# Kernel optimization log

Hardware: AMD Instinct MI355X
Metric: run time of the kernel (lower is better)

Reference implementation:

```python
import jax, jax.numpy as jnp
import numpy as np

N_NODES = 100000
N_EDGES = 1000000
D = 64


def _deg_inv_sqrt(idx, n):
    deg = jax.ops.segment_sum(jnp.ones(idx.shape[0], jnp.float32), idx, num_segments=n)
    deg = jnp.maximum(deg, 1.0)  # DGL clamps zero degrees to 1
    return jax.lax.rsqrt(deg)


def _graph_conv(x, W, b, src, dst, out_norm, in_norm):
    # norm='both': h = D_in^{-1/2} A D_out^{-1/2} x W + b
    h = x * out_norm[:, None]
    agg = jax.ops.segment_sum(h[src], dst, num_segments=x.shape[0])
    agg = agg * in_norm[:, None]
    return agg @ W + b


def setup_inputs() -> dict:
    key = jax.random.key(0)
    ks = jax.random.split(key, 8)
    x = jax.random.normal(ks[0], (N_NODES, D), dtype=jnp.float32)
    src = jax.random.randint(ks[1], (N_EDGES,), 0, N_NODES, dtype=jnp.int32)
    dst = jax.random.randint(ks[2], (N_EDGES,), 0, N_NODES, dtype=jnp.int32)
    s = 1.0 / np.sqrt(D)
    W1 = jax.random.normal(ks[3], (D, D), dtype=jnp.float32) * s
    W2 = jax.random.normal(ks[4], (D, D), dtype=jnp.float32) * s
    W3 = jax.random.normal(ks[5], (D, D), dtype=jnp.float32) * s
    b1 = jnp.zeros((D,), jnp.float32)
    b2 = jnp.zeros((D,), jnp.float32)
    b3 = jnp.zeros((D,), jnp.float32)
    return {"x": x, "src": src, "dst": dst,
            "W1": W1, "b1": b1, "W2": W2, "b2": b2, "W3": W3, "b3": b3}


def reference(x, src, dst, W1, b1, W2, b2, W3, b3):
    n = x.shape[0]
    out_norm = _deg_inv_sqrt(src, n)  # source out-degree norm
    in_norm = _deg_inv_sqrt(dst, n)   # dest in-degree norm
    h = _graph_conv(x, W1, b1, src, dst, out_norm, in_norm)
    h = jax.nn.relu(h)
    h = _graph_conv(h, W2, b2, src, dst, out_norm, in_norm)
    h = jax.nn.relu(h)
    h = _graph_conv(h, W3, b3, src, dst, out_norm, in_norm)
    return h
```

## Files before the change

kernel.cpp:

```cpp
#include <hip/hip_runtime.h>
#include <hip/hip_fp16.h>

#define D 64
#define SZ 512
#define EPB 4096
#define CAPB 8192

static __device__ __forceinline__ __half2 u2h2(unsigned u) {
    union { unsigned u; __half2 h; } c; c.u = u; return c.h;
}
static __device__ __forceinline__ unsigned h22u(__half2 h) {
    union { __half2 h; unsigned u; } c; c.h = h; return c.u;
}

__global__ __launch_bounds__(256) void scatter_kernel(
    const int* __restrict__ src, const int* __restrict__ dst,
    int* __restrict__ gcntD, int* __restrict__ gcntS,
    unsigned* __restrict__ packD, unsigned short* __restrict__ packS,
    int E, int nb) {
    int tid = threadIdx.x;
    __shared__ int hD[256], hS[256], baseD[256], baseS[256], curD[256], curS[256];
    hD[tid] = 0; hS[tid] = 0; curD[tid] = 0; curS[tid] = 0;
    __syncthreads();
    int ebase = (int)blockIdx.x * EPB;
#pragma unroll
    for (int k = 0; k < EPB / 256; k++) {
        int e = ebase + k * 256 + tid;
        if (e < E) {
            atomicAdd(&hD[dst[e] >> 9], 1);
            atomicAdd(&hS[src[e] >> 9], 1);
        }
    }
    __syncthreads();
    if (tid < nb) {
        int c = hD[tid];
        baseD[tid] = tid * CAPB + (c ? atomicAdd(&gcntD[tid], c) : 0);
        c = hS[tid];
        baseS[tid] = tid * CAPB + (c ? atomicAdd(&gcntS[tid], c) : 0);
    }
    __syncthreads();
#pragma unroll
    for (int k = 0; k < EPB / 256; k++) {
        int e = ebase + k * 256 + tid;
        if (e < E) {
            int s = src[e], d = dst[e];
            int bd = d >> 9, bs_ = s >> 9;
            int ld = atomicAdd(&curD[bd], 1);
            int ls = atomicAdd(&curS[bs_], 1);
            packD[baseD[bd] + ld] = ((unsigned)s << 9) | (unsigned)(d & 511);
            packS[baseS[bs_] + ls] = (unsigned short)(s & 511);
        }
    }
}

__global__ __launch_bounds__(256) void build_kernel(
    const unsigned* __restrict__ packD, const unsigned short* __restrict__ packS,
    const int* __restrict__ gcntD, const int* __restrict__ gcntS,
    int* __restrict__ csr, int* __restrict__ rowbeg, int* __restrict__ rowend,
    float* __restrict__ in_norm, float* __restrict__ out_norm,
    int n, int nb) {
    int tid = threadIdx.x;
    __shared__ int cnt[512], lptr[512], tmp[256];
    bool roleD = ((int)blockIdx.x < nb);
    int b = roleD ? (int)blockIdx.x : (int)blockIdx.x - nb;
    int bs = b * CAPB;
    int be = bs + (roleD ? gcntD[b] : gcntS[b]);
    cnt[tid] = 0; cnt[tid + 256] = 0;
    __syncthreads();
    if (roleD) {
        for (int i = bs + tid; i < be; i += 256)
            atomicAdd(&cnt[packD[i] & 511], 1);
        __syncthreads();
        int a0 = cnt[2 * tid], a1 = cnt[2 * tid + 1];
        tmp[tid] = a0 + a1; __syncthreads();
        for (int off = 1; off < 256; off <<= 1) {
            int u = (tid >= off) ? tmp[tid - off] : 0; __syncthreads();
            tmp[tid] += u; __syncthreads();
        }
        int ex = tmp[tid] - (a0 + a1);
        lptr[2 * tid] = ex; lptr[2 * tid + 1] = ex + a0;
        __syncthreads();
        int v0 = b * SZ + tid, v1 = v0 + 256;
        if (v0 < n) {
            rowbeg[v0] = bs + lptr[tid];
            rowend[v0] = bs + lptr[tid] + cnt[tid];
            in_norm[v0] = rsqrtf((float)max(cnt[tid], 1));
        }
        if (v1 < n) {
            rowbeg[v1] = bs + lptr[tid + 256];
            rowend[v1] = bs + lptr[tid + 256] + cnt[tid + 256];
            in_norm[v1] = rsqrtf((float)max(cnt[tid + 256], 1));
        }
        __syncthreads();
        for (int i = bs + tid; i < be; i += 256) {
            unsigned p = packD[i];
            int slot = atomicAdd(&lptr[p & 511], 1);
            csr[bs + slot] = (int)(p >> 9);
        }
    } else {
        for (int i = bs + tid; i < be; i += 256)
            atomicAdd(&cnt[packS[i]], 1);
        __syncthreads();
        int v0 = b * SZ + tid, v1 = v0 + 256;
        if (v0 < n) out_norm[v0] = rsqrtf((float)max(cnt[tid], 1));
        if (v1 < n) out_norm[v1] = rsqrtf((float)max(cnt[tid + 256], 1));
    }
}

template <int SCALE>
__global__ __launch_bounds__(256, 4) void gemm_kernel(
    const float* __restrict__ X, const float* __restrict__ W,
    const float* __restrict__ scale, __half* __restrict__ P, int n) {
    __shared__ float Ws[64 * 64];
    __shared__ float Xs[64 * 64];
    int tid = threadIdx.x;
    int row0 = (int)blockIdx.x * 64;
    if (row0 >= n) return;
    {
        const float4* W4 = (const float4*)W;
        float4* Ws4 = (float4*)Ws;
#pragma unroll
        for (int i = 0; i < 4; i++) Ws4[tid + 256 * i] = W4[tid + 256 * i];
    }
    {
#pragma unroll
        for (int i = 0; i < 4; i++) {
            int idx = tid + 256 * i;
            int r = idx >> 4, kq = idx & 15;
            float4 v = make_float4(0.f, 0.f, 0.f, 0.f);
            int row = row0 + r;
            if (row < n) v = ((const float4*)X)[(size_t)row * 16 + kq];
            *(float4*)&Xs[r * 64 + ((kq ^ (r & 15)) << 2)] = v;
        }
    }
    __syncthreads();

    int tx = tid & 15, ty = tid >> 4;
    float acc[4][4] = {};
#pragma unroll 4
    for (int kc = 0; kc < 16; kc++) {
        float4 wv[4];
#pragma unroll
        for (int j = 0; j < 4; j++) wv[j] = *(float4*)&Ws[(4 * kc + j) * 64 + 4 * tx];
#pragma unroll
        for (int r = 0; r < 4; r++) {
            int row = 4 * ty + r;
            float4 xv = *(float4*)&Xs[row * 64 + ((kc ^ (row & 15)) << 2)];
            acc[r][0] = fmaf(xv.x, wv[0].x, acc[r][0]);
            acc[r][1] = fmaf(xv.x, wv[0].y, acc[r][1]);
            acc[r][2] = fmaf(xv.x, wv[0].z, acc[r][2]);
            acc[r][3] = fmaf(xv.x, wv[0].w, acc[r][3]);
            acc[r][0] = fmaf(xv.y, wv[1].x, acc[r][0]);
            acc[r][1] = fmaf(xv.y, wv[1].y, acc[r][1]);
            acc[r][2] = fmaf(xv.y, wv[1].z, acc[r][2]);
            acc[r][3] = fmaf(xv.y, wv[1].w, acc[r][3]);
            acc[r][0] = fmaf(xv.z, wv[2].x, acc[r][0]);
            acc[r][1] = fmaf(xv.z, wv[2].y, acc[r][1]);
            acc[r][2] = fmaf(xv.z, wv[2].z, acc[r][2]);
            acc[r][3] = fmaf(xv.z, wv[2].w, acc[r][3]);
            acc[r][0] = fmaf(xv.w, wv[3].x, acc[r][0]);
            acc[r][1] = fmaf(xv.w, wv[3].y, acc[r][1]);
            acc[r][2] = fmaf(xv.w, wv[3].z, acc[r][2]);
            acc[r][3] = fmaf(xv.w, wv[3].w, acc[r][3]);
        }
    }
#pragma unroll
    for (int r = 0; r < 4; r++) {
        int row = row0 + 4 * ty + r;
        if (row < n) {
            float sc = SCALE ? scale[row] : 1.f;
            uint2 o;
            o.x = h22u(__floats2half2_rn(acc[r][0] * sc, acc[r][1] * sc));
            o.y = h22u(__floats2half2_rn(acc[r][2] * sc, acc[r][3] * sc));
            *(uint2*)&P[(size_t)row * 64 + 4 * tx] = o;
        }
    }
}

template <int RELU_SCALE>
__global__ __launch_bounds__(256) void gather_kernel(
    const uint4* __restrict__ P4, const int* __restrict__ csr,
    const int* __restrict__ rowbeg, const int* __restrict__ rowend,
    const float* __restrict__ in_norm, const float* __restrict__ out_norm,
    const float* __restrict__ bias, float4* __restrict__ out4, int n) {
    int tid = threadIdx.x;
    int g = tid & 7;
    int base_lane = tid & 56;
    int v = blockIdx.x * 32 + (tid >> 3);
    if (v >= n) return;

    int begin = rowbeg[v];
    int end = rowend[v];

    float inv = in_norm[v];
    float sc = RELU_SCALE ? out_norm[v] : 1.f;
    float4 blo = ((const float4*)bias)[2 * g];
    float4 bhi = ((const float4*)bias)[2 * g + 1];

    float al0 = 0.f, al1 = 0.f, al2 = 0.f, al3 = 0.f;
    float ah0 = 0.f, ah1 = 0.f, ah2 = 0.f, ah3 = 0.f;

    for (int e = begin; e < end; e += 8) {
        int ee = e + g;
        int jl = (ee < end) ? csr[ee] : -1;
        int js[8];
#pragma unroll
        for (int k = 0; k < 8; k++) js[k] = __shfl(jl, base_lane + k, 64);
        uint4 t[8];
#pragma unroll
        for (int k = 0; k < 8; k++) {
            t[k] = make_uint4(0u, 0u, 0u, 0u);
            if (js[k] >= 0) t[k] = P4[(size_t)js[k] * 8 + g];
        }
#pragma unroll
        for (int k = 0; k < 8; k++) {
            float2 f0 = __half22float2(u2h2(t[k].x));
            float2 f1 = __half22float2(u2h2(t[k].y));
            float2 f2 = __half22float2(u2h2(t[k].z));
            float2 f3 = __half22float2(u2h2(t[k].w));
            al0 += f0.x; al1 += f0.y; al2 += f1.x; al3 += f1.y;
            ah0 += f2.x; ah1 += f2.y; ah2 += f3.x; ah3 += f3.y;
        }
    }

    float4 o0, o1;
    o0.x = fmaf(al0, inv, blo.x); o0.y = fmaf(al1, inv, blo.y);
    o0.z = fmaf(al2, inv, blo.z); o0.w = fmaf(al3, inv, blo.w);
    o1.x = fmaf(ah0, inv, bhi.x); o1.y = fmaf(ah1, inv, bhi.y);
    o1.z = fmaf(ah2, inv, bhi.z); o1.w = fmaf(ah3, inv, bhi.w);
    if (RELU_SCALE) {
        o0.x = fmaxf(o0.x, 0.f) * sc; o0.y = fmaxf(o0.y, 0.f) * sc;
        o0.z = fmaxf(o0.z, 0.f) * sc; o0.w = fmaxf(o0.w, 0.f) * sc;
        o1.x = fmaxf(o1.x, 0.f) * sc; o1.y = fmaxf(o1.y, 0.f) * sc;
        o1.z = fmaxf(o1.z, 0.f) * sc; o1.w = fmaxf(o1.w, 0.f) * sc;
    }
    out4[(size_t)v * 16 + 2 * g] = o0;
    out4[(size_t)v * 16 + 2 * g + 1] = o1;
}


extern "C" void kernel_launch(void* const* d_in, const int* in_sizes, int n_in,
                              void* d_out, int out_size, void* d_ws, size_t ws_size,
                              hipStream_t stream) {
    const float* x  = (const float*)d_in[0];
    const int* src  = (const int*)d_in[1];
    const int* dst  = (const int*)d_in[2];
    const float* W1 = (const float*)d_in[3];
    const float* b1 = (const float*)d_in[4];
    const float* W2 = (const float*)d_in[5];
    const float* b2 = (const float*)d_in[6];
    const float* W3 = (const float*)d_in[7];
    const float* b3 = (const float*)d_in[8];

    const int N = in_sizes[0] / D;
    const int E = in_sizes[1];
    const int nb = (N + SZ - 1) / SZ;
    const int hb = (E + EPB - 1) / EPB;

    char* ws = (char*)d_ws;
    size_t off = 0;
    auto alloc = [&](size_t bytes) -> void* {
        void* p = (void*)(ws + off);
        off += (bytes + 15) & ~(size_t)15;
        return p;
    };
    int* gcntD = (int*)alloc(256 * 4);
    int* gcntS = (int*)alloc(256 * 4);
    unsigned* packD       = (unsigned*)alloc((size_t)nb * CAPB * 4);
    unsigned short* packS = (unsigned short*)alloc((size_t)nb * CAPB * 2);
    int* csr     = (int*)alloc((size_t)nb * CAPB * 4);
    int* rowbeg  = (int*)alloc((size_t)N * 4);
    int* rowend  = (int*)alloc((size_t)N * 4);
    float* innrm = (float*)alloc((size_t)N * 4);
    float* outnrm= (float*)alloc((size_t)N * 4);
    __half* bufP = (__half*)alloc((size_t)N * D * 2);
    float* bufH  = (float*)alloc((size_t)N * D * 4);

    const int gemmb = (N + 63) / 64;
    const int sgrid = (N + 31) / 32;

    hipMemsetAsync(gcntD, 0, 2 * 256 * sizeof(int), stream);

    scatter_kernel<<<hb, 256, 0, stream>>>(src, dst, gcntD, gcntS,
                                           packD, packS, E, nb);
    build_kernel<<<2 * nb, 256, 0, stream>>>(packD, packS, gcntD, gcntS, csr,
                                             rowbeg, rowend, innrm, outnrm, N, nb);

    gemm_kernel<1><<<gemmb, 256, 0, stream>>>(x, W1, outnrm, bufP, N);
    gather_kernel<1><<<sgrid, 256, 0, stream>>>((const uint4*)bufP, csr, rowbeg,
                                                rowend, innrm, outnrm, b1,
                                                (float4*)bufH, N);
    gemm_kernel<0><<<gemmb, 256, 0, stream>>>(bufH, W2, nullptr, bufP, N);
    gather_kernel<1><<<sgrid, 256, 0, stream>>>((const uint4*)bufP, csr, rowbeg,
                                                rowend, innrm, outnrm, b2,
                                                (float4*)bufH, N);
    gemm_kernel<0><<<gemmb, 256, 0, stream>>>(bufH, W3, nullptr, bufP, N);
    gather_kernel<0><<<sgrid, 256, 0, stream>>>((const uint4*)bufP, csr, rowbeg,
                                                rowend, innrm, outnrm, b3,
                                                (float4*)d_out, N);
}
```

Measured before the change: 243.9 us.

## Gather with one thread per node per feature quarter instead of 8-lane groups

The gather kernel now gives each thread a single destination node and one quarter of the feature dimension (16 halves, 32 bytes), with four blocks per 256-node range covering the feature quarters. Each thread reads its own CSR indices directly and issues two 16-byte loads per neighbor, so the wavefront shuffles are gone. The cost is that neighbouring lanes now read scattered rows rather than one contiguous 128-byte row. Lanes in a wavefront also see different degrees, so there is per-lane divergence, and each index is loaded four times.

Result: slower. 400.0 us (+64.0%).

```diff
diff --git a/kernel.cpp b/kernel.cpp
--- a/kernel.cpp
+++ b/kernel.cpp
@@ -184,58 +184,68 @@
     const float* __restrict__ in_norm, const float* __restrict__ out_norm,
     const float* __restrict__ bias, float4* __restrict__ out4, int n) {
     int tid = threadIdx.x;
-    int g = tid & 7;
-    int base_lane = tid & 56;
-    int v = blockIdx.x * 32 + (tid >> 3);
+    int fb = (int)blockIdx.x & 3;
+    int v = ((int)blockIdx.x >> 2) * 256 + tid;
     if (v >= n) return;
 
     int begin = rowbeg[v];
     int end = rowend[v];
-
     float inv = in_norm[v];
     float sc = RELU_SCALE ? out_norm[v] : 1.f;
-    float4 blo = ((const float4*)bias)[2 * g];
-    float4 bhi = ((const float4*)bias)[2 * g + 1];
-
-    float al0 = 0.f, al1 = 0.f, al2 = 0.f, al3 = 0.f;
-    float ah0 = 0.f, ah1 = 0.f, ah2 = 0.f, ah3 = 0.f;
-
-    for (int e = begin; e < end; e += 8) {
-        int ee = e + g;
-        int jl = (ee < end) ? csr[ee] : -1;
-        int js[8];
-#pragma unroll
-        for (int k = 0; k < 8; k++) js[k] = __shfl(jl, base_lane + k, 64);
+
+    const uint4* Pb = P4 + 2 * fb;
+
+    float a[16];
+#pragma unroll
+    for (int q = 0; q < 16; q++) a[q] = 0.f;
+
+    for (int e = begin; e < end; e += 4) {
+        int j[4];
+#pragma unroll
+        for (int i = 0; i < 4; i++) {
+            int ee = e + i;
+            j[i] = (ee < end) ? csr[ee] : -1;
+        }
         uint4 t[8];
 #pragma unroll
-        for (int k = 0; k < 8; k++) {
-            t[k] = make_uint4(0u, 0u, 0u, 0u);
-            if (js[k] >= 0) t[k] = P4[(size_t)js[k] * 8 + g];
-        }
-#pragma unroll
-        for (int k = 0; k < 8; k++) {
-            float2 f0 = __half22float2(u2h2(t[k].x));
-            float2 f1 = __half22float2(u2h2(t[k].y));
-            float2 f2 = __half22float2(u2h2(t[k].z));
-            float2 f3 = __half22float2(u2h2(t[k].w));
-            al0 += f0.x; al1 += f0.y; al2 += f1.x; al3 += f1.y;
-            ah0 += f2.x; ah1 += f2.y; ah2 += f3.x; ah3 += f3.y;
-        }
-    }
-
-    float4 o0, o1;
-    o0.x = fmaf(al0, inv, blo.x); o0.y = fmaf(al1, inv, blo.y);
-    o0.z = fmaf(al2, inv, blo.z); o0.w = fmaf(al3, inv, blo.w);
-    o1.x = fmaf(ah0, inv, bhi.x); o1.y = fmaf(ah1, inv, bhi.y);
-    o1.z = fmaf(ah2, inv, bhi.z); o1.w = fmaf(ah3, inv, bhi.w);
-    if (RELU_SCALE) {
-        o0.x = fmaxf(o0.x, 0.f) * sc; o0.y = fmaxf(o0.y, 0.f) * sc;
-        o0.z = fmaxf(o0.z, 0.f) * sc; o0.w = fmaxf(o0.w, 0.f) * sc;
-        o1.x = fmaxf(o1.x, 0.f) * sc; o1.y = fmaxf(o1.y, 0.f) * sc;
-        o1.z = fmaxf(o1.z, 0.f) * sc; o1.w = fmaxf(o1.w, 0.f) * sc;
-    }
-    out4[(size_t)v * 16 + 2 * g] = o0;
-    out4[(size_t)v * 16 + 2 * g + 1] = o1;
+        for (int i = 0; i < 4; i++) {
+            t[2 * i] = make_uint4(0u, 0u, 0u, 0u);
+            t[2 * i + 1] = make_uint4(0u, 0u, 0u, 0u);
+            if (j[i] >= 0) {
+                const uint4* p = Pb + (size_t)j[i] * 8;
+                t[2 * i] = p[0];
+                t[2 * i + 1] = p[1];
+            }
+        }
+#pragma unroll
+        for (int i = 0; i < 8; i++) {
+            float2 f0 = __half22float2(u2h2(t[i].x));
+            float2 f1 = __half22float2(u2h2(t[i].y));
+            float2 f2 = __half22float2(u2h2(t[i].z));
+            float2 f3 = __half22float2(u2h2(t[i].w));
+            int o = (i & 1) * 8;
+            a[o + 0] += f0.x; a[o + 1] += f0.y;
+            a[o + 2] += f1.x; a[o + 3] += f1.y;
+            a[o + 4] += f2.x; a[o + 5] += f2.y;
+            a[o + 6] += f3.x; a[o + 7] += f3.y;
+        }
+    }
+
+    const float4* b4 = (const float4*)bias + 4 * fb;
+#pragma unroll
+    for (int q = 0; q < 4; q++) {
+        float4 bq = b4[q];
+        float4 o;
+        o.x = fmaf(a[4 * q + 0], inv, bq.x);
+        o.y = fmaf(a[4 * q + 1], inv, bq.y);
+        o.z = fmaf(a[4 * q + 2], inv, bq.z);
+        o.w = fmaf(a[4 * q + 3], inv, bq.w);
+        if (RELU_SCALE) {
+            o.x = fmaxf(o.x, 0.f) * sc; o.y = fmaxf(o.y, 0.f) * sc;
+            o.z = fmaxf(o.z, 0.f) * sc; o.w = fmaxf(o.w, 0.f) * sc;
+        }
+        out4[(size_t)v * 16 + 4 * fb + q] = o;
+    }
 }
 
 
@@ -277,7 +287,7 @@
     float* bufH  = (float*)alloc((size_t)N * D * 4);
 
     const int gemmb = (N + 63) / 64;
-    const int sgrid = (N + 31) / 32;
+    const int sgrid = ((N + 255) / 256) * 4;
 
     hipMemsetAsync(gcntD, 0, 2 * 256 * sizeof(int), stream);
 
```

## Fuse gather with next-layer GEMM and stage edges in shared memory

Applied to the files above, without the earlier changes.

Layers 1 and 2 now run a combined kernel: it aggregates neighbour rows, applies bias, ReLU and the out-degree scale, keeps the 32 resulting rows in shared memory, multiplies them by the next weight matrix and writes fp16 projections directly. This drops the fp32 intermediate buffer round trip and two GEMM launches. Separately, the scatter kernel caches each block's src/dst edges in shared memory so the second pass does not reread global memory, and the edges per block shrink from 4096 to 1024, giving more blocks. In exchange, every gather block reloads the 16KB weight matrix, and the fused GEMM has less register reuse than the tiled GEMM.

Measured after the change: 241.6 us. Within noise of the previous version (-1.0%).

```diff
diff --git a/kernel.cpp b/kernel.cpp
--- a/kernel.cpp
+++ b/kernel.cpp
@@ -3,7 +3,7 @@
 
 #define D 64
 #define SZ 512
-#define EPB 4096
+#define EPB 1024
 #define CAPB 8192
 
 static __device__ __forceinline__ __half2 u2h2(unsigned u) {
@@ -20,15 +20,20 @@
     int E, int nb) {
     int tid = threadIdx.x;
     __shared__ int hD[256], hS[256], baseD[256], baseS[256], curD[256], curS[256];
+    __shared__ int es[EPB], ed[EPB];
     hD[tid] = 0; hS[tid] = 0; curD[tid] = 0; curS[tid] = 0;
     __syncthreads();
     int ebase = (int)blockIdx.x * EPB;
 #pragma unroll
     for (int k = 0; k < EPB / 256; k++) {
         int e = ebase + k * 256 + tid;
-        if (e < E) {
-            atomicAdd(&hD[dst[e] >> 9], 1);
-            atomicAdd(&hS[src[e] >> 9], 1);
+        int s = -1, d = 0;
+        if (e < E) { s = src[e]; d = dst[e]; }
+        es[k * 256 + tid] = s;
+        ed[k * 256 + tid] = d;
+        if (s >= 0) {
+            atomicAdd(&hD[d >> 9], 1);
+            atomicAdd(&hS[s >> 9], 1);
         }
     }
     __syncthreads();
@@ -41,9 +46,9 @@
     __syncthreads();
 #pragma unroll
     for (int k = 0; k < EPB / 256; k++) {
-        int e = ebase + k * 256 + tid;
-        if (e < E) {
-            int s = src[e], d = dst[e];
+        int s = es[k * 256 + tid];
+        if (s >= 0) {
+            int d = ed[k * 256 + tid];
             int bd = d >> 9, bs_ = s >> 9;
             int ld = atomicAdd(&curD[bd], 1);
             int ls = atomicAdd(&curS[bs_], 1);
@@ -107,7 +112,6 @@
     }
 }
 
-template <int SCALE>
 __global__ __launch_bounds__(256, 4) void gemm_kernel(
     const float* __restrict__ X, const float* __restrict__ W,
     const float* __restrict__ scale, __half* __restrict__ P, int n) {
@@ -168,7 +172,7 @@
     for (int r = 0; r < 4; r++) {
         int row = row0 + 4 * ty + r;
         if (row < n) {
-            float sc = SCALE ? scale[row] : 1.f;
+            float sc = scale[row];
             uint2 o;
             o.x = h22u(__floats2half2_rn(acc[r][0] * sc, acc[r][1] * sc));
             o.y = h22u(__floats2half2_rn(acc[r][2] * sc, acc[r][3] * sc));
@@ -177,12 +181,98 @@
     }
 }
 
-template <int RELU_SCALE>
+__global__ __launch_bounds__(256) void gather_gemm_kernel(
+    const uint4* __restrict__ P4, const int* __restrict__ csr,
+    const int* __restrict__ rowbeg, const int* __restrict__ rowend,
+    const float* __restrict__ in_norm, const float* __restrict__ out_norm,
+    const float* __restrict__ bias, const float* __restrict__ W,
+    __half* __restrict__ Pout, int n) {
+    __shared__ float Ws[64 * 64];
+    __shared__ float Hs[32 * 64];
+    int tid = threadIdx.x;
+    {
+        const float4* W4 = (const float4*)W;
+        float4* Ws4 = (float4*)Ws;
+#pragma unroll
+        for (int i = 0; i < 4; i++) Ws4[tid + 256 * i] = W4[tid + 256 * i];
+    }
+    int g = tid & 7;
+    int base_lane = tid & 56;
+    int vl = tid >> 3;
+    int v = (int)blockIdx.x * 32 + vl;
+    bool act = (v < n);
+
+    if (act) {
+        int begin = rowbeg[v];
+        int end = rowend[v];
+        float al0 = 0.f, al1 = 0.f, al2 = 0.f, al3 = 0.f;
+        float ah0 = 0.f, ah1 = 0.f, ah2 = 0.f, ah3 = 0.f;
+        for (int e = begin; e < end; e += 8) {
+            int ee = e + g;
+            int jl = (ee < end) ? csr[ee] : -1;
+            int js[8];
+#pragma unroll
+            for (int k = 0; k < 8; k++) js[k] = __shfl(jl, base_lane + k, 64);
+            uint4 t[8];
+#pragma unroll
+            for (int k = 0; k < 8; k++) {
+                t[k] = make_uint4(0u, 0u, 0u, 0u);
+                if (js[k] >= 0) t[k] = P4[(size_t)js[k] * 8 + g];
+            }
+#pragma unroll
+            for (int k = 0; k < 8; k++) {
+                float2 f0 = __half22float2(u2h2(t[k].x));
+                float2 f1 = __half22float2(u2h2(t[k].y));
+                float2 f2 = __half22float2(u2h2(t[k].z));
+                float2 f3 = __half22float2(u2h2(t[k].w));
+                al0 += f0.x; al1 += f0.y; al2 += f1.x; al3 += f1.y;
+                ah0 += f2.x; ah1 += f2.y; ah2 += f3.x; ah3 += f3.y;
+            }
+        }
+        float inv = in_norm[v];
+        float sc = out_norm[v];
+        float4 blo = ((const float4*)bias)[2 * g];
+        float4 bhi = ((const float4*)bias)[2 * g + 1];
+        float4 h0, h1;
+        h0.x = fmaxf(fmaf(al0, inv, blo.x), 0.f) * sc;
+        h0.y = fmaxf(fmaf(al1, inv, blo.y), 0.f) * sc;
+        h0.z = fmaxf(fmaf(al2, inv, blo.z), 0.f) * sc;
+        h0.w = fmaxf(fmaf(al3, inv, blo.w), 0.f) * sc;
+        h1.x = fmaxf(fmaf(ah0, inv, bhi.x), 0.f) * sc;
+        h1.y = fmaxf(fmaf(ah1, inv, bhi.y), 0.f) * sc;
+        h1.z = fmaxf(fmaf(ah2, inv, bhi.z), 0.f) * sc;
+        h1.w = fmaxf(fmaf(ah3, inv, bhi.w), 0.f) * sc;
+        *(float4*)&Hs[vl * 64 + 8 * g] = h0;
+        *(float4*)&Hs[vl * 64 + 8 * g + 4] = h1;
+    }
+    __syncthreads();
+    if (act) {
+        float4 o0 = make_float4(0.f, 0.f, 0.f, 0.f);
+        float4 o1 = make_float4(0.f, 0.f, 0.f, 0.f);
+#pragma unroll 8
+        for (int k = 0; k < 64; k++) {
+            float h = Hs[vl * 64 + k];
+            float4 w0 = *(float4*)&Ws[k * 64 + 8 * g];
+            float4 w1 = *(float4*)&Ws[k * 64 + 8 * g + 4];
+            o0.x = fmaf(h, w0.x, o0.x); o0.y = fmaf(h, w0.y, o0.y);
+            o0.z = fmaf(h, w0.z, o0.z); o0.w = fmaf(h, w0.w, o0.w);
+            o1.x = fmaf(h, w1.x, o1.x); o1.y = fmaf(h, w1.y, o1.y);
+            o1.z = fmaf(h, w1.z, o1.z); o1.w = fmaf(h, w1.w, o1.w);
+        }
+        uint4 t;
+        t.x = h22u(__floats2half2_rn(o0.x, o0.y));
+        t.y = h22u(__floats2half2_rn(o0.z, o0.w));
+        t.z = h22u(__floats2half2_rn(o1.x, o1.y));
+        t.w = h22u(__floats2half2_rn(o1.z, o1.w));
+        ((uint4*)Pout)[(size_t)v * 8 + g] = t;
+    }
+}
+
 __global__ __launch_bounds__(256) void gather_kernel(
     const uint4* __restrict__ P4, const int* __restrict__ csr,
     const int* __restrict__ rowbeg, const int* __restrict__ rowend,
-    const float* __restrict__ in_norm, const float* __restrict__ out_norm,
-    const float* __restrict__ bias, float4* __restrict__ out4, int n) {
+    const float* __restrict__ in_norm, const float* __restrict__ bias,
+    float4* __restrict__ out4, int n) {
     int tid = threadIdx.x;
     int g = tid & 7;
     int base_lane = tid & 56;
@@ -191,9 +281,7 @@
 
     int begin = rowbeg[v];
     int end = rowend[v];
-
     float inv = in_norm[v];
-    float sc = RELU_SCALE ? out_norm[v] : 1.f;
     float4 blo = ((const float4*)bias)[2 * g];
     float4 bhi = ((const float4*)bias)[2 * g + 1];
 
@@ -228,12 +316,6 @@
     o0.z = fmaf(al2, inv, blo.z); o0.w = fmaf(al3, inv, blo.w);
     o1.x = fmaf(ah0, inv, bhi.x); o1.y = fmaf(ah1, inv, bhi.y);
     o1.z = fmaf(ah2, inv, bhi.z); o1.w = fmaf(ah3, inv, bhi.w);
-    if (RELU_SCALE) {
-        o0.x = fmaxf(o0.x, 0.f) * sc; o0.y = fmaxf(o0.y, 0.f) * sc;
-        o0.z = fmaxf(o0.z, 0.f) * sc; o0.w = fmaxf(o0.w, 0.f) * sc;
-        o1.x = fmaxf(o1.x, 0.f) * sc; o1.y = fmaxf(o1.y, 0.f) * sc;
-        o1.z = fmaxf(o1.z, 0.f) * sc; o1.w = fmaxf(o1.w, 0.f) * sc;
-    }
     out4[(size_t)v * 16 + 2 * g] = o0;
     out4[(size_t)v * 16 + 2 * g + 1] = o1;
 }
@@ -273,8 +355,8 @@
     int* rowend  = (int*)alloc((size_t)N * 4);
     float* innrm = (float*)alloc((size_t)N * 4);
     float* outnrm= (float*)alloc((size_t)N * 4);
-    __half* bufP = (__half*)alloc((size_t)N * D * 2);
-    float* bufH  = (float*)alloc((size_t)N * D * 4);
+    __half* bufPa = (__half*)alloc((size_t)N * D * 2);
+    __half* bufPb = (__half*)alloc((size_t)N * D * 2);
 
     const int gemmb = (N + 63) / 64;
     const int sgrid = (N + 31) / 32;
@@ -286,16 +368,13 @@
     build_kernel<<<2 * nb, 256, 0, stream>>>(packD, packS, gcntD, gcntS, csr,
                                              rowbeg, rowend, innrm, outnrm, N, nb);
 
-    gemm_kernel<1><<<gemmb, 256, 0, stream>>>(x, W1, outnrm, bufP, N);
-    gather_kernel<1><<<sgrid, 256, 0, stream>>>((const uint4*)bufP, csr, rowbeg,
-                                                rowend, innrm, outnrm, b1,
-                                                (float4*)bufH, N);
-    gemm_kernel<0><<<gemmb, 256, 0, stream>>>(bufH, W2, nullptr, bufP, N);
-    gather_kernel<1><<<sgrid, 256, 0, stream>>>((const uint4*)bufP, csr, rowbeg,
-                                                rowend, innrm, outnrm, b2,
-                                                (float4*)bufH, N);
-    gemm_kernel<0><<<gemmb, 256, 0, stream>>>(bufH, W3, nullptr, bufP, N);
-    gather_kernel<0><<<sgrid, 256, 0, stream>>>((const uint4*)bufP, csr, rowbeg,
-                                                rowend, innrm, outnrm, b3,
-                                                (float4*)d_out, N);
-}
+    gemm_kernel<<<gemmb, 256, 0, stream>>>(x, W1, outnrm, bufPa, N);
+    gather_gemm_kernel<<<sgrid, 256, 0, stream>>>((const uint4*)bufPa, csr, rowbeg,
+                                                  rowend, innrm, outnrm, b1, W2,
+                                                  bufPb, N);
+    gather_gemm_kernel<<<sgrid, 256, 0, stream>>>((const uint4*)bufPb, csr, rowbeg,
+                                                  rowend, innrm, outnrm, b2, W3,
+                                                  bufPa, N);
+    gather_kernel<<<sgrid, 256, 0, stream>>>((const uint4*)bufPa, csr, rowbeg,
+                                             rowend, innrm, b3, (float4*)d_out, N);
+}
```
